# Kernel tuning notes

Measured on AMD Instinct MI355X. Metric: run time of the kernel, lower is better.

## Reference

```python
import jax, jax.numpy as jnp
import numpy as np

N_HEADS = 16
D_HEAD = 64
D_MODEL = 1024
WINDOW = 256
B, T = 4, 2048


def rotate_half(x):
    x1, x2 = jnp.split(x, 2, axis=-1)
    return jnp.concatenate([-x2, x1], axis=-1)


def apply_rope(x, cos, sin):
    return x * cos + rotate_half(x) * sin


def setup_inputs() -> dict:
    key = jax.random.key(0)
    ks = jax.random.split(key, 5)
    x = jax.random.normal(ks[0], (B, T, D_MODEL), dtype=jnp.float32)
    cos = jax.random.normal(ks[1], (1, T, 1, D_HEAD), dtype=jnp.float32)
    sin = jax.random.normal(ks[2], (1, T, 1, D_HEAD), dtype=jnp.float32)
    qkv_w = jax.random.normal(ks[3], (3 * D_MODEL, D_MODEL), dtype=jnp.float32) * (D_MODEL ** -0.5)
    out_w = jax.random.normal(ks[4], (D_MODEL, D_MODEL), dtype=jnp.float32) * (D_MODEL ** -0.5)
    return {"x": x, "cos": cos, "sin": sin, "qkv_w": qkv_w, "out_w": out_w}


def reference(x, cos, sin, qkv_w, out_w):
    Bc, Tc, C = x.shape
    # QKV projection (bias-free Linear: y = x @ W^T)
    qkv = jnp.einsum('btc,fc->btf', x, qkv_w)
    q, k, v = jnp.split(qkv, 3, axis=-1)
    # [B, H, T, d]
    def to_heads(t):
        return t.reshape(Bc, Tc, N_HEADS, D_HEAD).transpose(0, 2, 1, 3)
    q, k, v = to_heads(q), to_heads(k), to_heads(v)
    # RoPE: cos/sin [1, T, 1, d] -> [1, 1, T, d] broadcasting over heads
    cos_t = cos[:, :Tc].transpose(0, 2, 1, 3)
    sin_t = sin[:, :Tc].transpose(0, 2, 1, 3)
    q = apply_rope(q, cos_t, sin_t)
    k = apply_rope(k, cos_t, sin_t)
    # banded causal mask: allow j <= i and j >= i - (window-1)
    i = jnp.arange(Tc)[:, None]
    j = jnp.arange(Tc)[None, :]
    allowed = (j <= i) & (j >= i - (WINDOW - 1))  # [T, T]
    scale = 1.0 / jnp.sqrt(jnp.asarray(D_HEAD, dtype=q.dtype))
    scores = jnp.einsum('bhqd,bhkd->bhqk', q, k) * scale
    scores = jnp.where(allowed[None, None], scores, jnp.finfo(scores.dtype).min)
    attn = jax.nn.softmax(scores, axis=-1)
    out = jnp.einsum('bhqk,bhkd->bhqd', attn, v)
    out = out.transpose(0, 2, 1, 3).reshape(Bc, Tc, C)
    return jnp.einsum('btc,oc->bto', out, out_w)
```

## Files before the change

kernel.cpp:

```cpp
#include <hip/hip_runtime.h>

typedef __bf16 bf16_t;
typedef __bf16 bf16x8 __attribute__((ext_vector_type(8)));
typedef __bf16 bf16x4 __attribute__((ext_vector_type(4)));
typedef float f32x4 __attribute__((ext_vector_type(4)));

#define GLOAD_LDS16(gptr, lptr)                                                              \
  __builtin_amdgcn_global_load_lds((const __attribute__((address_space(1))) void*)(gptr),    \
                                   (__attribute__((address_space(3))) void*)(lptr), 16, 0, 0)

__device__ __forceinline__ f32x4 f32x4_zero() {
  f32x4 v; v[0] = 0.f; v[1] = 0.f; v[2] = 0.f; v[3] = 0.f; return v;
}

__device__ __forceinline__ int kxr(int r) { return (r & 7) ^ (((r >> 3) & 3) << 1); }

__global__ void cast3_kernel(const float* __restrict__ a, const float* __restrict__ b,
                             const float* __restrict__ c, bf16_t* __restrict__ oa,
                             bf16_t* __restrict__ ob, bf16_t* __restrict__ oc) {
  int i = blockIdx.x * blockDim.x + threadIdx.x;
  const float* src; bf16_t* dst; int j;
  if (i < 2097152) { src = a; dst = oa; j = i; }
  else if (i < 2883584) { src = b; dst = ob; j = i - 2097152; }
  else { src = c; dst = oc; j = i - 2883584; }
  float4 v = ((const float4*)src)[j];
  bf16x4 o;
  o[0] = (bf16_t)v.x; o[1] = (bf16_t)v.y; o[2] = (bf16_t)v.z; o[3] = (bf16_t)v.w;
  ((bf16x4*)dst)[j] = o;
}

template <int MODE>
__global__ __launch_bounds__(256) void gemm_bt_kernel(
    const bf16_t* __restrict__ A, const bf16_t* __restrict__ B, float* __restrict__ C,
    bf16_t* __restrict__ oq, bf16_t* __restrict__ ok_, bf16_t* __restrict__ ov,
    int M, int N, int K) {
  constexpr int BM = 128, BN = 128, BK = 32;
  __shared__ bf16_t As[BM * BK];
  __shared__ bf16_t Bs[BN * BK];
  const int tid = threadIdx.x;
  const int lane = tid & 63;
  const int wid = tid >> 6;
  const int wm = (wid >> 1) * 64;
  const int wn = (wid & 1) * 64;
  const int l16 = lane & 15;
  const int qd = lane >> 4;
  const int bm = blockIdx.x, bn = blockIdx.y;

  const int srow = tid >> 2;
  const int skol = (tid & 3) * 8;

  const bf16_t* gA = A + (size_t)(bm * BM + srow) * K + skol;
  const bf16_t* gB = B + (size_t)(bn * BN + srow) * K + skol;
  bf16_t* lA = &As[srow * BK + skol];
  bf16_t* lB = &Bs[srow * BK + skol];

  f32x4 acc[4][4];
#pragma unroll
  for (int mb = 0; mb < 4; mb++)
#pragma unroll
    for (int nb = 0; nb < 4; nb++) acc[mb][nb] = f32x4_zero();

  for (int k0 = 0; k0 < K; k0 += BK) {
    __syncthreads();
    GLOAD_LDS16(gA + k0, lA);
    GLOAD_LDS16(gA + (size_t)64 * K + k0, lA + 64 * BK);
    GLOAD_LDS16(gB + k0, lB);
    GLOAD_LDS16(gB + (size_t)64 * K + k0, lB + 64 * BK);
    __syncthreads();

    bf16x8 af[4], bfr[4];
#pragma unroll
    for (int mb = 0; mb < 4; mb++)
      af[mb] = *(const bf16x8*)&As[(wm + mb * 16 + l16) * BK + qd * 8];
#pragma unroll
    for (int nb = 0; nb < 4; nb++)
      bfr[nb] = *(const bf16x8*)&Bs[(wn + nb * 16 + l16) * BK + qd * 8];
#pragma unroll
    for (int mb = 0; mb < 4; mb++)
#pragma unroll
      for (int nb = 0; nb < 4; nb++)
        acc[mb][nb] = __builtin_amdgcn_mfma_f32_16x16x32_bf16(af[mb], bfr[nb], acc[mb][nb], 0, 0, 0);
  }

  if (MODE == 0) {
#pragma unroll
    for (int mb = 0; mb < 4; mb++)
#pragma unroll
      for (int nb = 0; nb < 4; nb++)
#pragma unroll
        for (int r = 0; r < 4; r++) {
          int row = bm * BM + wm + mb * 16 + qd * 4 + r;
          int col = bn * BN + wn + nb * 16 + l16;
          C[(size_t)row * N + col] = acc[mb][nb][r];
        }
  } else {
    const int part = bn >> 3;
    const int h = ((bn * 128 + wn) & 1023) >> 6;
    bf16_t* dst = (part == 0) ? oq : (part == 1) ? ok_ : ov;
#pragma unroll
    for (int mb = 0; mb < 4; mb++)
#pragma unroll
      for (int r = 0; r < 4; r++) {
        int row = bm * BM + wm + mb * 16 + qd * 4 + r;
        int b = row >> 11, t = row & 2047;
        size_t basei = (((size_t)(b * 16 + h)) * 2048 + t) * 64;
#pragma unroll
        for (int nb = 0; nb < 4; nb++)
          dst[basei + nb * 16 + l16] = (bf16_t)acc[mb][nb][r];
      }
  }
}

__device__ __forceinline__ void rope_tile_lds(bf16_t* buf, const float* __restrict__ cosp,
                                              const float* __restrict__ sinp, int tbase,
                                              int tid, float sc) {
#pragma unroll
  for (int p2 = 0; p2 < 2; p2++) {
    int it = p2 * 256 + tid;
    int r = it >> 3, pq = it & 7;
    int d0 = pq * 4;
    int t = tbase + r;
    int a_lo = (r * 8 + ((d0 >> 3) ^ (r & 7))) * 8 + (d0 & 7);
    int a_hi = (r * 8 + (((d0 + 32) >> 3) ^ (r & 7))) * 8 + (d0 & 7);
    bf16x4 xl = *(bf16x4*)&buf[a_lo];
    bf16x4 xh = *(bf16x4*)&buf[a_hi];
    float4 cl = *(const float4*)&cosp[t * 64 + d0];
    float4 ch = *(const float4*)&cosp[t * 64 + d0 + 32];
    float4 sl = *(const float4*)&sinp[t * 64 + d0];
    float4 sh = *(const float4*)&sinp[t * 64 + d0 + 32];
    bf16x4 ol, oh;
    ol[0] = (bf16_t)(((float)xl[0] * cl.x - (float)xh[0] * sl.x) * sc);
    ol[1] = (bf16_t)(((float)xl[1] * cl.y - (float)xh[1] * sl.y) * sc);
    ol[2] = (bf16_t)(((float)xl[2] * cl.z - (float)xh[2] * sl.z) * sc);
    ol[3] = (bf16_t)(((float)xl[3] * cl.w - (float)xh[3] * sl.w) * sc);
    oh[0] = (bf16_t)(((float)xh[0] * ch.x + (float)xl[0] * sh.x) * sc);
    oh[1] = (bf16_t)(((float)xh[1] * ch.y + (float)xl[1] * sh.y) * sc);
    oh[2] = (bf16_t)(((float)xh[2] * ch.z + (float)xl[2] * sh.z) * sc);
    oh[3] = (bf16_t)(((float)xh[3] * ch.w + (float)xl[3] * sh.w) * sc);
    *(bf16x4*)&buf[a_lo] = ol;
    *(bf16x4*)&buf[a_hi] = oh;
  }
}

__global__ __launch_bounds__(256) void attn_kernel(
    const bf16_t* __restrict__ qh, const bf16_t* __restrict__ kh,
    const bf16_t* __restrict__ vh, bf16_t* __restrict__ ao,
    const float* __restrict__ cosp, const float* __restrict__ sinp) {
  __shared__ bf16_t qs[64 * 64];
  __shared__ bf16_t ks[64 * 64];
  __shared__ bf16_t vs[64 * 64];
  __shared__ bf16_t vswz[8 * 64 * 8];
  __shared__ bf16_t ps[4][16 * 64];

  const int tid = threadIdx.x;
  const int lane = tid & 63;
  const int wid = tid >> 6;
  const int l16 = lane & 15;
  const int qd = lane >> 4;

  const int bh = blockIdx.x;
  const int i0 = blockIdx.y * 64;
  const int b = bh >> 4, h = bh & 15;

  auto swz4 = [](int f) { int r = f >> 3; return r * 8 + ((f & 7) ^ (r & 7)); };
  const int r0 = tid >> 3, q0 = tid & 7;

  {
    const uint4* src = (const uint4*)(qh + ((size_t)bh * 2048 + i0) * 64);
    uint4* dst = (uint4*)qs;
    dst[swz4(tid)] = src[tid];
    dst[swz4(tid + 256)] = src[tid + 256];
  }
  __syncthreads();
  rope_tile_lds(qs, cosp, sinp, i0, tid, 0.18033688011112042f);

  bf16x8 bones;
#pragma unroll
  for (int e = 0; e < 8; e++) bones[e] = (bf16_t)1.0f;

  float l_i[4] = {0.f, 0.f, 0.f, 0.f};
  f32x4 oacc[4];
#pragma unroll
  for (int nb = 0; nb < 4; nb++) oacc[nb] = f32x4_zero();

  const int c1 = i0 >> 6;
  const int c0 = (c1 >= 4) ? (c1 - 4) : 0;

  for (int c = c0; c <= c1; c++) {
    const int j0 = c * 64;
    __syncthreads();
    {
      const uint4* ksrc = (const uint4*)(kh + ((size_t)bh * 2048 + j0) * 64);
      const uint4* vsrc = (const uint4*)(vh + ((size_t)bh * 2048 + j0) * 64);
      uint4* kdst = (uint4*)ks; uint4* vdst = (uint4*)vs;
      kdst[swz4(tid)] = ksrc[tid]; kdst[swz4(tid + 256)] = ksrc[tid + 256];
      vdst[r0 * 8 + (q0 ^ kxr(r0))] = vsrc[tid];
      vdst[(r0 + 32) * 8 + (q0 ^ kxr(r0 + 32))] = vsrc[tid + 256];
    }
    __syncthreads();
    rope_tile_lds(ks, cosp, sinp, j0, tid, 1.0f);
    __syncthreads();

    f32x4 sacc[4];
#pragma unroll
    for (int nb = 0; nb < 4; nb++) sacc[nb] = f32x4_zero();
#pragma unroll
    for (int kk = 0; kk < 2; kk++) {
      bf16x8 afr = *(const bf16x8*)&qs[(wid * 16 + l16) * 64 + (((kk * 4 + qd) ^ (l16 & 7)) * 8)];
#pragma unroll
      for (int nb = 0; nb < 4; nb++) {
        bf16x8 bfr = *(const bf16x8*)&ks[(nb * 16 + l16) * 64 + (((kk * 4 + qd) ^ (l16 & 7)) * 8)];
        sacc[nb] = __builtin_amdgcn_mfma_f32_16x16x32_bf16(afr, bfr, sacc[nb], 0, 0, 0);
      }
    }

#pragma unroll
    for (int p2 = 0; p2 < 2; p2++) {
      int combo = p2 * 4 + wid;
      int jbase = (combo >> 2) * 32 + (lane >> 4) * 8;
      int dcol = (combo & 3) * 16 + (lane & 15);
      int bb = dcol >> 3, dlo = dcol & 7;
      bf16x8 v8;
#pragma unroll
      for (int e = 0; e < 8; e++) {
        int row = jbase + e;
        v8[e] = vs[row * 64 + ((bb ^ kxr(row)) * 8) + dlo];
      }
      *(bf16x8*)&vswz[(combo * 64 + lane) * 8] = v8;
    }

#pragma unroll
    for (int r = 0; r < 4; r++) {
      const int i = i0 + wid * 16 + qd * 4 + r;
      const int prow = qd * 4 + r;
#pragma unroll
      for (int nb = 0; nb < 4; nb++) {
        const int j = j0 + nb * 16 + l16;
        bool valid = (j <= i) && (j + 256 > i);
        float p = valid ? exp2f(sacc[nb][r]) : 0.f;
        ps[wid][prow * 64 + (((nb * 2 + (l16 >> 3)) ^ (prow & 7)) * 8) + (l16 & 7)] = (bf16_t)p;
      }
    }

    __syncthreads();

    f32x4 lacc = f32x4_zero();
#pragma unroll
    for (int kk = 0; kk < 2; kk++) {
      bf16x8 afr = *(const bf16x8*)&ps[wid][l16 * 64 + (((kk * 4 + qd) ^ (l16 & 7)) * 8)];
      lacc = __builtin_amdgcn_mfma_f32_16x16x32_bf16(afr, bones, lacc, 0, 0, 0);
#pragma unroll
      for (int nb = 0; nb < 4; nb++) {
        bf16x8 bfr = *(const bf16x8*)&vswz[((kk * 4 + nb) * 64 + lane) * 8];
        oacc[nb] = __builtin_amdgcn_mfma_f32_16x16x32_bf16(afr, bfr, oacc[nb], 0, 0, 0);
      }
    }
#pragma unroll
    for (int r = 0; r < 4; r++) l_i[r] += lacc[r];
  }

#pragma unroll
  for (int nb = 0; nb < 4; nb++) {
#pragma unroll
    for (int r = 0; r < 4; r++) {
      int t = i0 + wid * 16 + qd * 4 + r;
      ao[((size_t)(b * 2048 + t)) * 1024 + h * 64 + nb * 16 + l16] =
          (bf16_t)(oacc[nb][r] / l_i[r]);
    }
  }
}

extern "C" void kernel_launch(void* const* d_in, const int* in_sizes, int n_in,
                              void* d_out, int out_size, void* d_ws, size_t ws_size,
                              hipStream_t stream) {
  const float* x    = (const float*)d_in[0];
  const float* cosp = (const float*)d_in[1];
  const float* sinp = (const float*)d_in[2];
  const float* qkvw = (const float*)d_in[3];
  const float* outw = (const float*)d_in[4];
  float* out = (float*)d_out;

  char* ws = (char*)d_ws;
  bf16_t* xb  = (bf16_t*)(ws + 0);
  bf16_t* qwb = (bf16_t*)(ws + 16777216);
  bf16_t* owb = (bf16_t*)(ws + 23068672);
  bf16_t* qhp = (bf16_t*)(ws + 25165824);
  bf16_t* khp = (bf16_t*)(ws + 41943040);
  bf16_t* vhp = (bf16_t*)(ws + 58720256);
  bf16_t* aop = (bf16_t*)(ws + 75497472);

  cast3_kernel<<<12288, 256, 0, stream>>>(x, qkvw, outw, xb, qwb, owb);

  gemm_bt_kernel<1><<<dim3(64, 24), 256, 0, stream>>>(xb, qwb, nullptr, qhp, khp, vhp,
                                                      8192, 3072, 1024);
  attn_kernel<<<dim3(64, 32), 256, 0, stream>>>(qhp, khp, vhp, aop, cosp, sinp);
  gemm_bt_kernel<0><<<dim3(64, 8), 256, 0, stream>>>(aop, owb, out, nullptr, nullptr, nullptr,
                                                     8192, 1024, 1024);
}
```

Baseline: 234.7 us.

## Hoist RoPE into separate pass and double query rows per attention block

RoPE is moved out of the attention kernel into its own elementwise pass over Q and K. Each K tile is therefore no longer rotated again by every query block that reads it, and one barrier per chunk goes away. The attention block now covers 128 query rows, with each wave holding two 16-row fragments in registers, so each K/V chunk load feeds twice as many MFMAs. The P buffer reuses the Q shared-memory area, and launch bounds request 3 blocks per CU. The costs are an extra read-write pass over Q/K in global memory, one extra K/V chunk per block from the wider window, and higher register pressure.

```diff
diff --git a/kernel.cpp b/kernel.cpp
--- a/kernel.cpp
+++ b/kernel.cpp
@@ -111,46 +111,43 @@
   }
 }
 
-__device__ __forceinline__ void rope_tile_lds(bf16_t* buf, const float* __restrict__ cosp,
-                                              const float* __restrict__ sinp, int tbase,
-                                              int tid, float sc) {
-#pragma unroll
-  for (int p2 = 0; p2 < 2; p2++) {
-    int it = p2 * 256 + tid;
-    int r = it >> 3, pq = it & 7;
-    int d0 = pq * 4;
-    int t = tbase + r;
-    int a_lo = (r * 8 + ((d0 >> 3) ^ (r & 7))) * 8 + (d0 & 7);
-    int a_hi = (r * 8 + (((d0 + 32) >> 3) ^ (r & 7))) * 8 + (d0 & 7);
-    bf16x4 xl = *(bf16x4*)&buf[a_lo];
-    bf16x4 xh = *(bf16x4*)&buf[a_hi];
-    float4 cl = *(const float4*)&cosp[t * 64 + d0];
-    float4 ch = *(const float4*)&cosp[t * 64 + d0 + 32];
-    float4 sl = *(const float4*)&sinp[t * 64 + d0];
-    float4 sh = *(const float4*)&sinp[t * 64 + d0 + 32];
-    bf16x4 ol, oh;
-    ol[0] = (bf16_t)(((float)xl[0] * cl.x - (float)xh[0] * sl.x) * sc);
-    ol[1] = (bf16_t)(((float)xl[1] * cl.y - (float)xh[1] * sl.y) * sc);
-    ol[2] = (bf16_t)(((float)xl[2] * cl.z - (float)xh[2] * sl.z) * sc);
-    ol[3] = (bf16_t)(((float)xl[3] * cl.w - (float)xh[3] * sl.w) * sc);
-    oh[0] = (bf16_t)(((float)xh[0] * ch.x + (float)xl[0] * sh.x) * sc);
-    oh[1] = (bf16_t)(((float)xh[1] * ch.y + (float)xl[1] * sh.y) * sc);
-    oh[2] = (bf16_t)(((float)xh[2] * ch.z + (float)xl[2] * sh.z) * sc);
-    oh[3] = (bf16_t)(((float)xh[3] * ch.w + (float)xl[3] * sh.w) * sc);
-    *(bf16x4*)&buf[a_lo] = ol;
-    *(bf16x4*)&buf[a_hi] = oh;
-  }
-}
-
-__global__ __launch_bounds__(256) void attn_kernel(
+__global__ void ropeqk_kernel(bf16_t* __restrict__ qh, bf16_t* __restrict__ kh,
+                              const float* __restrict__ cosp, const float* __restrict__ sinp) {
+  int gid = blockIdx.x * 256 + threadIdx.x;
+  bool isq = gid < 1048576;
+  int ii = gid & 1048575;
+  bf16_t* ptr = isq ? qh : kh;
+  const float sc = isq ? 0.18033688011112042f : 1.0f;
+  int d0 = (ii & 7) * 4;
+  int t = (ii >> 3) & 2047;
+  int bh = ii >> 14;
+  size_t base = ((size_t)bh * 2048 + t) * 64;
+  bf16x4 lo = *(bf16x4*)&ptr[base + d0];
+  bf16x4 hi = *(bf16x4*)&ptr[base + d0 + 32];
+  float4 cl = *(const float4*)&cosp[t * 64 + d0];
+  float4 ch = *(const float4*)&cosp[t * 64 + d0 + 32];
+  float4 sl = *(const float4*)&sinp[t * 64 + d0];
+  float4 sh = *(const float4*)&sinp[t * 64 + d0 + 32];
+  bf16x4 ol, oh;
+  ol[0] = (bf16_t)(((float)lo[0] * cl.x - (float)hi[0] * sl.x) * sc);
+  ol[1] = (bf16_t)(((float)lo[1] * cl.y - (float)hi[1] * sl.y) * sc);
+  ol[2] = (bf16_t)(((float)lo[2] * cl.z - (float)hi[2] * sl.z) * sc);
+  ol[3] = (bf16_t)(((float)lo[3] * cl.w - (float)hi[3] * sl.w) * sc);
+  oh[0] = (bf16_t)(((float)hi[0] * ch.x + (float)lo[0] * sh.x) * sc);
+  oh[1] = (bf16_t)(((float)hi[1] * ch.y + (float)lo[1] * sh.y) * sc);
+  oh[2] = (bf16_t)(((float)hi[2] * ch.z + (float)lo[2] * sh.z) * sc);
+  oh[3] = (bf16_t)(((float)hi[3] * ch.w + (float)lo[3] * sh.w) * sc);
+  *(bf16x4*)&ptr[base + d0] = ol;
+  *(bf16x4*)&ptr[base + d0 + 32] = oh;
+}
+
+__global__ __launch_bounds__(256, 3) void attn_kernel(
     const bf16_t* __restrict__ qh, const bf16_t* __restrict__ kh,
-    const bf16_t* __restrict__ vh, bf16_t* __restrict__ ao,
-    const float* __restrict__ cosp, const float* __restrict__ sinp) {
-  __shared__ bf16_t qs[64 * 64];
+    const bf16_t* __restrict__ vh, bf16_t* __restrict__ ao) {
+  __shared__ bf16_t qps[128 * 64];
   __shared__ bf16_t ks[64 * 64];
   __shared__ bf16_t vs[64 * 64];
   __shared__ bf16_t vswz[8 * 64 * 8];
-  __shared__ bf16_t ps[4][16 * 64];
 
   const int tid = threadIdx.x;
   const int lane = tid & 63;
@@ -159,58 +156,71 @@
   const int qd = lane >> 4;
 
   const int bh = blockIdx.x;
-  const int i0 = blockIdx.y * 64;
+  const int i0 = blockIdx.y * 128;
   const int b = bh >> 4, h = bh & 15;
-
-  auto swz4 = [](int f) { int r = f >> 3; return r * 8 + ((f & 7) ^ (r & 7)); };
   const int r0 = tid >> 3, q0 = tid & 7;
 
   {
-    const uint4* src = (const uint4*)(qh + ((size_t)bh * 2048 + i0) * 64);
-    uint4* dst = (uint4*)qs;
-    dst[swz4(tid)] = src[tid];
-    dst[swz4(tid + 256)] = src[tid + 256];
+    const uint4* qsrc = (const uint4*)(qh + ((size_t)bh * 2048 + i0) * 64);
+    uint4* q4 = (uint4*)qps;
+#pragma unroll
+    for (int p = 0; p < 4; p++) {
+      int f = p * 256 + tid, rr = f >> 3;
+      q4[rr * 8 + ((f & 7) ^ (rr & 7))] = qsrc[f];
+    }
   }
   __syncthreads();
-  rope_tile_lds(qs, cosp, sinp, i0, tid, 0.18033688011112042f);
+
+  bf16x8 qfrag[2][2];
+#pragma unroll
+  for (int mb = 0; mb < 2; mb++)
+#pragma unroll
+    for (int kk = 0; kk < 2; kk++) {
+      int row = wid * 32 + mb * 16 + l16;
+      qfrag[mb][kk] = *(const bf16x8*)&qps[row * 64 + (((kk * 4 + qd) ^ (l16 & 7)) * 8)];
+    }
 
   bf16x8 bones;
 #pragma unroll
   for (int e = 0; e < 8; e++) bones[e] = (bf16_t)1.0f;
 
-  float l_i[4] = {0.f, 0.f, 0.f, 0.f};
-  f32x4 oacc[4];
-#pragma unroll
-  for (int nb = 0; nb < 4; nb++) oacc[nb] = f32x4_zero();
-
-  const int c1 = i0 >> 6;
-  const int c0 = (c1 >= 4) ? (c1 - 4) : 0;
+  float l_i[2][4] = {{0.f, 0.f, 0.f, 0.f}, {0.f, 0.f, 0.f, 0.f}};
+  f32x4 oacc[2][4];
+#pragma unroll
+  for (int mb = 0; mb < 2; mb++)
+#pragma unroll
+    for (int nb = 0; nb < 4; nb++) oacc[mb][nb] = f32x4_zero();
+
+  const int ct = i0 >> 6;
+  const int c1 = ct + 1;
+  const int c0 = (ct >= 4) ? (ct - 4) : 0;
+  const uint4* ksrc = (const uint4*)(kh + (size_t)bh * 2048 * 64);
+  const uint4* vsrc = (const uint4*)(vh + (size_t)bh * 2048 * 64);
+  uint4* k4 = (uint4*)ks;
+  uint4* v4 = (uint4*)vs;
 
   for (int c = c0; c <= c1; c++) {
     const int j0 = c * 64;
     __syncthreads();
-    {
-      const uint4* ksrc = (const uint4*)(kh + ((size_t)bh * 2048 + j0) * 64);
-      const uint4* vsrc = (const uint4*)(vh + ((size_t)bh * 2048 + j0) * 64);
-      uint4* kdst = (uint4*)ks; uint4* vdst = (uint4*)vs;
-      kdst[swz4(tid)] = ksrc[tid]; kdst[swz4(tid + 256)] = ksrc[tid + 256];
-      vdst[r0 * 8 + (q0 ^ kxr(r0))] = vsrc[tid];
-      vdst[(r0 + 32) * 8 + (q0 ^ kxr(r0 + 32))] = vsrc[tid + 256];
-    }
-    __syncthreads();
-    rope_tile_lds(ks, cosp, sinp, j0, tid, 1.0f);
-    __syncthreads();
-
-    f32x4 sacc[4];
-#pragma unroll
-    for (int nb = 0; nb < 4; nb++) sacc[nb] = f32x4_zero();
+    k4[r0 * 8 + (q0 ^ (r0 & 7))] = ksrc[c * 512 + tid];
+    k4[(r0 + 32) * 8 + (q0 ^ ((r0 + 32) & 7))] = ksrc[c * 512 + tid + 256];
+    v4[r0 * 8 + (q0 ^ kxr(r0))] = vsrc[c * 512 + tid];
+    v4[(r0 + 32) * 8 + (q0 ^ kxr(r0 + 32))] = vsrc[c * 512 + tid + 256];
+    __syncthreads();
+
+    f32x4 sacc[2][4];
+#pragma unroll
+    for (int mb = 0; mb < 2; mb++)
+#pragma unroll
+      for (int nb = 0; nb < 4; nb++) sacc[mb][nb] = f32x4_zero();
 #pragma unroll
     for (int kk = 0; kk < 2; kk++) {
-      bf16x8 afr = *(const bf16x8*)&qs[(wid * 16 + l16) * 64 + (((kk * 4 + qd) ^ (l16 & 7)) * 8)];
 #pragma unroll
       for (int nb = 0; nb < 4; nb++) {
-        bf16x8 bfr = *(const bf16x8*)&ks[(nb * 16 + l16) * 64 + (((kk * 4 + qd) ^ (l16 & 7)) * 8)];
-        sacc[nb] = __builtin_amdgcn_mfma_f32_16x16x32_bf16(afr, bfr, sacc[nb], 0, 0, 0);
+        int brow = nb * 16 + l16;
+        bf16x8 bfr = *(const bf16x8*)&ks[brow * 64 + (((kk * 4 + qd) ^ (brow & 7)) * 8)];
+        sacc[0][nb] = __builtin_amdgcn_mfma_f32_16x16x32_bf16(qfrag[0][kk], bfr, sacc[0][nb], 0, 0, 0);
+        sacc[1][nb] = __builtin_amdgcn_mfma_f32_16x16x32_bf16(qfrag[1][kk], bfr, sacc[1][nb], 0, 0, 0);
       }
     }
 
@@ -230,44 +240,54 @@
     }
 
 #pragma unroll
-    for (int r = 0; r < 4; r++) {
-      const int i = i0 + wid * 16 + qd * 4 + r;
-      const int prow = qd * 4 + r;
-#pragma unroll
-      for (int nb = 0; nb < 4; nb++) {
-        const int j = j0 + nb * 16 + l16;
-        bool valid = (j <= i) && (j + 256 > i);
-        float p = valid ? exp2f(sacc[nb][r]) : 0.f;
-        ps[wid][prow * 64 + (((nb * 2 + (l16 >> 3)) ^ (prow & 7)) * 8) + (l16 & 7)] = (bf16_t)p;
-      }
-    }
-
-    __syncthreads();
-
-    f32x4 lacc = f32x4_zero();
+    for (int mb = 0; mb < 2; mb++)
+#pragma unroll
+      for (int r = 0; r < 4; r++) {
+        const int i = i0 + wid * 32 + mb * 16 + qd * 4 + r;
+        const int prow = qd * 4 + r;
+        const int rowp = wid * 32 + mb * 16 + prow;
+#pragma unroll
+        for (int nb = 0; nb < 4; nb++) {
+          const int j = j0 + nb * 16 + l16;
+          bool valid = (j <= i) && (j + 256 > i);
+          float p = valid ? exp2f(sacc[mb][nb][r]) : 0.f;
+          qps[rowp * 64 + (((nb * 2 + (l16 >> 3)) ^ (prow & 7)) * 8) + (l16 & 7)] = (bf16_t)p;
+        }
+      }
+
+    __syncthreads();
+
+    f32x4 lacc[2];
+    lacc[0] = f32x4_zero(); lacc[1] = f32x4_zero();
 #pragma unroll
     for (int kk = 0; kk < 2; kk++) {
-      bf16x8 afr = *(const bf16x8*)&ps[wid][l16 * 64 + (((kk * 4 + qd) ^ (l16 & 7)) * 8)];
-      lacc = __builtin_amdgcn_mfma_f32_16x16x32_bf16(afr, bones, lacc, 0, 0, 0);
+      bf16x8 afr0 = *(const bf16x8*)&qps[(wid * 32 + l16) * 64 + (((kk * 4 + qd) ^ (l16 & 7)) * 8)];
+      bf16x8 afr1 = *(const bf16x8*)&qps[(wid * 32 + 16 + l16) * 64 + (((kk * 4 + qd) ^ (l16 & 7)) * 8)];
+      lacc[0] = __builtin_amdgcn_mfma_f32_16x16x32_bf16(afr0, bones, lacc[0], 0, 0, 0);
+      lacc[1] = __builtin_amdgcn_mfma_f32_16x16x32_bf16(afr1, bones, lacc[1], 0, 0, 0);
 #pragma unroll
       for (int nb = 0; nb < 4; nb++) {
         bf16x8 bfr = *(const bf16x8*)&vswz[((kk * 4 + nb) * 64 + lane) * 8];
-        oacc[nb] = __builtin_amdgcn_mfma_f32_16x16x32_bf16(afr, bfr, oacc[nb], 0, 0, 0);
-      }
-    }
-#pragma unroll
-    for (int r = 0; r < 4; r++) l_i[r] += lacc[r];
+        oacc[0][nb] = __builtin_amdgcn_mfma_f32_16x16x32_bf16(afr0, bfr, oacc[0][nb], 0, 0, 0);
+        oacc[1][nb] = __builtin_amdgcn_mfma_f32_16x16x32_bf16(afr1, bfr, oacc[1][nb], 0, 0, 0);
+      }
+    }
+#pragma unroll
+    for (int mb = 0; mb < 2; mb++)
+#pragma unroll
+      for (int r = 0; r < 4; r++) l_i[mb][r] += lacc[mb][r];
   }
 
 #pragma unroll
-  for (int nb = 0; nb < 4; nb++) {
-#pragma unroll
-    for (int r = 0; r < 4; r++) {
-      int t = i0 + wid * 16 + qd * 4 + r;
-      ao[((size_t)(b * 2048 + t)) * 1024 + h * 64 + nb * 16 + l16] =
-          (bf16_t)(oacc[nb][r] / l_i[r]);
-    }
-  }
+  for (int mb = 0; mb < 2; mb++)
+#pragma unroll
+    for (int nb = 0; nb < 4; nb++)
+#pragma unroll
+      for (int r = 0; r < 4; r++) {
+        int t = i0 + wid * 32 + mb * 16 + qd * 4 + r;
+        ao[((size_t)(b * 2048 + t)) * 1024 + h * 64 + nb * 16 + l16] =
+            (bf16_t)(oacc[mb][nb][r] / l_i[mb][r]);
+      }
 }
 
 extern "C" void kernel_launch(void* const* d_in, const int* in_sizes, int n_in,
@@ -293,7 +313,8 @@
 
   gemm_bt_kernel<1><<<dim3(64, 24), 256, 0, stream>>>(xb, qwb, nullptr, qhp, khp, vhp,
                                                       8192, 3072, 1024);
-  attn_kernel<<<dim3(64, 32), 256, 0, stream>>>(qhp, khp, vhp, aop, cosp, sinp);
+  ropeqk_kernel<<<8192, 256, 0, stream>>>(qhp, khp, cosp, sinp);
+  attn_kernel<<<dim3(64, 16), 256, 0, stream>>>(qhp, khp, vhp, aop);
   gemm_bt_kernel<0><<<dim3(64, 8), 256, 0, stream>>>(aop, owb, out, nullptr, nullptr, nullptr,
                                                      8192, 1024, 1024);
 }
```

New measurement: 255.9 us. 9.0% more time.
